# Kernel optimization log

Hardware: AMD Instinct MI355X
Metric: run time of the kernel (lower is better)

Reference implementation:

```python
import jax, jax.numpy as jnp
import numpy as np

ATOM_FDIM, BOND_FDIM, HID, DEPTH = 133, 147, 256, 4
N_ATOMS, N_BONDS, MAX_NB, A_PER_MOL = 4096, 8192, 6, 64


def _ln(x, g, b, eps=1e-5):
    mu = x.mean(-1, keepdims=True)
    var = ((x - mu) ** 2).mean(-1, keepdims=True)
    return (x - mu) / jnp.sqrt(var + eps) * g + b


def setup_inputs() -> dict:
    key = jax.random.key(0)
    ks = jax.random.split(key, 20)
    def w(k, i, o):
        return jax.random.normal(k, (i, o), jnp.float32) / np.sqrt(i).astype(np.float32)
    return {
        "f_atoms": jax.random.normal(ks[0], (N_ATOMS, ATOM_FDIM), jnp.float32),
        "f_bonds": jax.random.normal(ks[1], (N_BONDS, BOND_FDIM), jnp.float32),
        "Wq_atom": w(ks[2], ATOM_FDIM, ATOM_FDIM),
        "Wk_atom": w(ks[3], ATOM_FDIM, ATOM_FDIM),
        "Wv_atom": w(ks[4], ATOM_FDIM, ATOM_FDIM),
        "ln_g": jnp.ones((ATOM_FDIM,), jnp.float32),
        "ln_b": jnp.zeros((ATOM_FDIM,), jnp.float32),
        "Wi": w(ks[5], BOND_FDIM, HID),
        "Wh": w(ks[6], HID, HID),
        "Wq": w(ks[7], HID, HID),
        "Wk": w(ks[8], HID, HID),
        "Wv": w(ks[9], HID, HID),
        "Wa": w(ks[10], HID, HID),
        "Walpha_w": w(ks[11], 2 * HID, 1),
        "Walpha_b": jnp.zeros((1,), jnp.float32),
        "Wo_w": w(ks[12], ATOM_FDIM + HID, HID),
        "Wo_b": jnp.zeros((HID,), jnp.float32),
        "Wb_w": w(ks[13], HID, HID),
        "Wb_b": jnp.zeros((HID,), jnp.float32),
        "a2b": jax.random.randint(ks[14], (N_ATOMS, MAX_NB), 0, N_BONDS),
        "b2a": jax.random.randint(ks[15], (N_BONDS,), 0, N_ATOMS),
        "b2revb": jax.random.randint(ks[16], (N_BONDS,), 0, N_BONDS),
        "atoms_per_mol": A_PER_MOL,
    }


def reference(f_atoms, f_bonds, Wq_atom, Wk_atom, Wv_atom, ln_g, ln_b, Wi, Wh,
              Wq, Wk, Wv, Wa, Walpha_w, Walpha_b, Wo_w, Wo_b, Wb_w, Wb_b,
              a2b, b2a, b2revb, atoms_per_mol):
    M = f_atoms.shape[0] // atoms_per_mol
    fdim = f_atoms.shape[1]
    # --- per-molecule atom self-attention enhancement (uniform a_scope) ---
    x = f_atoms.reshape(M, atoms_per_mol, fdim)  # [M, A, F]
    q, k, v = x @ Wq_atom, x @ Wk_atom, x @ Wv_atom
    scores = jnp.einsum('maf,mbf->mab', q, k) / np.sqrt(fdim).astype(np.float32)
    attn_out = jnp.einsum('mab,mbf->maf', jax.nn.softmax(scores, -1), v)
    f_atoms_e = _ln(x + attn_out, ln_g, ln_b).reshape(-1, fdim)

    # --- bond message init ---
    inputs = f_bonds @ Wi                      # [B, H]
    message = jax.nn.relu(inputs)
    sqrt_h = np.sqrt(HID).astype(np.float32)

    for _ in range(DEPTH - 1):
        # DMPNN gather-sum
        a_message = message[a2b].sum(1)        # [N_atoms, H]
        dmpnn = (a_message[b2a] - message[b2revb]) @ Wh
        # global bond-bond attention (faithful to torch: over all messages)
        Q, K, V = message @ Wq, message @ Wk, message @ Wv
        att_w = jax.nn.softmax(Q @ K.T / sqrt_h, -1)   # [B, B]
        att_msg = (att_w @ V) @ Wa
        alpha = jax.nn.sigmoid(
            jnp.concatenate([dmpnn, att_msg], -1) @ Walpha_w + Walpha_b)
        message = jax.nn.relu(inputs + alpha * dmpnn + (1.0 - alpha) * att_msg)
        # dropout is identity in eval mode

    # --- atom readout ---
    a_message = message[a2b].sum(1)
    a_input = jnp.concatenate([f_atoms_e, a_message], 1)
    atom_h = jax.nn.relu(a_input @ Wo_w + Wo_b)        # [N_atoms, H]

    # --- per-molecule attentive pooling ---
    hm = atom_h.reshape(M, atoms_per_mol, HID)
    aw = jax.nn.softmax(jnp.einsum('mah,mbh->mab', hm @ Wa, hm), -1)
    att_h = jax.nn.relu(jnp.einsum('mab,mbh->mah', aw, hm) @ Wb_w + Wb_b)
    mol_vecs = (hm + att_h).sum(1) / atoms_per_mol
    return mol_vecs
```

## Files before the change

kernel.cpp:

```cpp
#include <hip/hip_runtime.h>
#include <hip/hip_bf16.h>

typedef __hip_bfloat16 hbf16;
typedef __bf16 bf16x8 __attribute__((ext_vector_type(8)));
typedef float floatx4 __attribute__((ext_vector_type(4)));

#define N_ATOMS 4096
#define N_BONDS 8192
#define FDIM 133
#define BFDIM 147
#define HID 256
#define APM 64
#define NMOL 64
#define FA_S 160
#define FB_S 160
#define AI_S 416

struct P4 { float* p[4]; };
struct CvtTab { const void* src[6]; float* dst[6]; int n[6]; };
struct WTab { const void* src[11]; hbf16* dst[11]; int K[11]; int Hout[11]; int Kp[11]; int total[11]; };

__device__ __forceinline__ float bcvt(hbf16 x) { return __bfloat162float(x); }

__device__ __forceinline__ float load_in(const void* src, int i, int f32flag)
{
    return f32flag ? ((const float*)src)[i] : bcvt(((const hbf16*)src)[i]);
}

__device__ __forceinline__ void split8(const float4 a0, const float4 a1,
                                       bf16x8& hi, bf16x8& lo)
{
    const float v[8] = {a0.x, a0.y, a0.z, a0.w, a1.x, a1.y, a1.z, a1.w};
    #pragma unroll
    for (int i = 0; i < 8; i++) {
        const __bf16 h = (__bf16)v[i];
        hi[i] = h;
        lo[i] = (__bf16)(v[i] - (float)h);
    }
}

__global__ void detect_kernel(const unsigned short* __restrict__ probe, int* __restrict__ flag)
{
    const int t = threadIdx.x;
    float mx = 0.f;
    for (int i = t; i < 4096; i += 64) {
        unsigned int u = ((unsigned int)probe[i]) << 16;
        float v;
        __builtin_memcpy(&v, &u, 4);
        v = fabsf(v);
        if (!(v == v)) v = 0.f;
        if (v > 1e6f) v = 1e6f;
        mx = fmaxf(mx, v);
    }
    #pragma unroll
    for (int o = 32; o > 0; o >>= 1) mx = fmaxf(mx, __shfl_xor(mx, o));
    if (t == 0) *flag = (mx > 100.f) ? 1 : 0;
}

__global__ void small_cvt_kernel(CvtTab tab, const int* __restrict__ flag)
{
    const int f32 = *flag;
    for (int s = 0; s < 6; s++)
        for (int i = threadIdx.x; i < tab.n[s]; i += 256)
            tab.dst[s][i] = load_in(tab.src[s], i, f32);
}

__global__ void cvt_pad_kernel(const void* __restrict__ src, float* __restrict__ dst,
                               int N, int K, int Kp, const int* __restrict__ flag)
{
    const int i = blockIdx.x * 256 + threadIdx.x;
    if (i >= N * Kp) return;
    const int r = i / Kp, k = i - r * Kp;
    dst[i] = (k < K) ? load_in(src, r * K + k, *flag) : 0.f;
}

__global__ void wt_all_kernel(WTab tab, const int* __restrict__ flag)
{
    const int wid = blockIdx.y;
    const int f32 = *flag;
    const int tot = tab.total[wid], Kp = tab.Kp[wid], K = tab.K[wid], Hout = tab.Hout[wid];
    hbf16* dst = tab.dst[wid];
    const void* src = tab.src[wid];
    for (int i = blockIdx.x * 256 + threadIdx.x; i < tot; i += gridDim.x * 256) {
        const int n = i / Kp, k = i - n * Kp;
        const float v = (k < K && n < Hout) ? load_in(src, k * Hout + n, f32) : 0.f;
        dst[i] = __float2bfloat16(v);
    }
}

__global__ __launch_bounds__(256)
void mgemm_kernel(const float* __restrict__ A, int lda, const hbf16* __restrict__ Wt,
                  const float* __restrict__ bias,
                  float* __restrict__ Cf, float* __restrict__ Cf2, int ldcf,
                  hbf16* __restrict__ Cbh, hbf16* __restrict__ Cbl, int ldcb,
                  hbf16* __restrict__ CbT, int ldct,
                  int Hout, int HoutStore, int relu)
{
    const int t = threadIdx.x, w = t >> 6, ln = t & 63;
    const int lane16 = ln & 15, quad = ln >> 4;
    const int rb = blockIdx.y * 64 + w * 16, cb = blockIdx.x * 64;
    const floatx4 zero4 = {0.f, 0.f, 0.f, 0.f};
    floatx4 acc[4] = {zero4, zero4, zero4, zero4};
    const float* ar = A + (size_t)(rb + lane16) * lda + quad * 8;
    for (int kk = 0; kk < lda; kk += 32) {
        const float4 a0 = *(const float4*)(ar + kk);
        const float4 a1 = *(const float4*)(ar + kk + 4);
        bf16x8 af;
        af[0] = (__bf16)a0.x; af[1] = (__bf16)a0.y; af[2] = (__bf16)a0.z; af[3] = (__bf16)a0.w;
        af[4] = (__bf16)a1.x; af[5] = (__bf16)a1.y; af[6] = (__bf16)a1.z; af[7] = (__bf16)a1.w;
        #pragma unroll
        for (int nt = 0; nt < 4; nt++) {
            const bf16x8 bf =
                *(const bf16x8*)&Wt[(size_t)(cb + nt * 16 + lane16) * lda + kk + quad * 8];
            acc[nt] = __builtin_amdgcn_mfma_f32_16x16x32_bf16(af, bf, acc[nt], 0, 0, 0);
        }
    }
    #pragma unroll
    for (int nt = 0; nt < 4; nt++) {
        const int n = cb + nt * 16 + lane16;
        if (n >= HoutStore) continue;
        const bool valid = n < Hout;
        const float bv = (bias && valid) ? bias[n] : 0.f;
        #pragma unroll
        for (int r = 0; r < 4; r++) {
            const int m = rb + quad * 4 + r;
            float v = valid ? acc[nt][r] + bv : 0.f;
            if (relu) v = fmaxf(v, 0.f);
            if (Cf)  Cf[(size_t)m * ldcf + n] = v;
            if (Cf2) Cf2[(size_t)m * ldcf + n] = fmaxf(v, 0.f);
            if (Cbh) {
                const hbf16 h = __float2bfloat16(v);
                Cbh[(size_t)m * ldcb + n] = h;
                if (Cbl) Cbl[(size_t)m * ldcb + n] = __float2bfloat16(v - bcvt(h));
            }
            if (CbT) CbT[(size_t)n * ldct + m] = __float2bfloat16(v);
        }
    }
}

__global__ __launch_bounds__(256)
void atom_fused_kernel(const float* __restrict__ qa, const float* __restrict__ ka,
                       const hbf16* __restrict__ vT, const float* __restrict__ f_atoms_p,
                       const float* __restrict__ ln_g, const float* __restrict__ ln_b,
                       float* __restrict__ f_e)
{
    __shared__ float S[64][68];
    __shared__ __bf16 P[64][72];
    __shared__ float Y[64][136];
    const int m = blockIdx.x, t = threadIdx.x;
    const int w = t >> 6, ln = t & 63;
    const int lane16 = ln & 15, quad = ln >> 4;
    const int base = m * APM;
    const floatx4 zero4 = {0.f, 0.f, 0.f, 0.f};

    {
        floatx4 acc[4] = {zero4, zero4, zero4, zero4};
        const float* arow = qa + (size_t)(base + w * 16 + lane16) * FA_S + quad * 8;
        #pragma unroll
        for (int ks = 0; ks < 5; ks++) {
            bf16x8 ah, al;
            split8(*(const float4*)(arow + ks * 32), *(const float4*)(arow + ks * 32 + 4), ah, al);
            #pragma unroll
            for (int nt = 0; nt < 4; nt++) {
                const float* brow = ka + (size_t)(base + nt * 16 + lane16) * FA_S + ks * 32 + quad * 8;
                bf16x8 bh, bl;
                split8(*(const float4*)brow, *(const float4*)(brow + 4), bh, bl);
                acc[nt] = __builtin_amdgcn_mfma_f32_16x16x32_bf16(ah, bh, acc[nt], 0, 0, 0);
                acc[nt] = __builtin_amdgcn_mfma_f32_16x16x32_bf16(al, bh, acc[nt], 0, 0, 0);
                acc[nt] = __builtin_amdgcn_mfma_f32_16x16x32_bf16(ah, bl, acc[nt], 0, 0, 0);
            }
        }
        const float scale = 1.f / sqrtf(133.f);
        #pragma unroll
        for (int nt = 0; nt < 4; nt++)
            #pragma unroll
            for (int r = 0; r < 4; r++)
                S[w * 16 + quad * 4 + r][nt * 16 + lane16] = acc[nt][r] * scale;
    }
    for (int r = w * 16; r < w * 16 + 16; r++) {
        const float x = S[r][ln];
        float mx = x;
        #pragma unroll
        for (int o = 32; o > 0; o >>= 1) mx = fmaxf(mx, __shfl_xor(mx, o));
        const float p = __expf(x - mx);
        float sm = p;
        #pragma unroll
        for (int o = 32; o > 0; o >>= 1) sm += __shfl_xor(sm, o);
        P[r][ln] = (__bf16)(p / sm);
    }
    {
        floatx4 o[9];
        #pragma unroll
        for (int i = 0; i < 9; i++) o[i] = zero4;
        #pragma unroll
        for (int ks = 0; ks < 2; ks++) {
            const bf16x8 af = *(const bf16x8*)&P[w * 16 + lane16][ks * 32 + quad * 8];
            #pragma unroll
            for (int nt = 0; nt < 9; nt++) {
                const bf16x8 bfv =
                    *(const bf16x8*)&vT[(size_t)(nt * 16 + lane16) * N_ATOMS + base + ks * 32 + quad * 8];
                o[nt] = __builtin_amdgcn_mfma_f32_16x16x32_bf16(af, bfv, o[nt], 0, 0, 0);
            }
        }
        #pragma unroll
        for (int nt = 0; nt < 9; nt++) {
            const int f = nt * 16 + lane16;
            if (f >= FDIM) continue;
            #pragma unroll
            for (int r = 0; r < 4; r++) {
                const int a = w * 16 + quad * 4 + r;
                Y[a][f] = f_atoms_p[(size_t)(base + a) * FA_S + f] + o[nt][r];
            }
        }
    }
    for (int r = w * 16; r < w * 16 + 16; r++) {
        float sum = 0.f, sq = 0.f;
        for (int f = ln; f < FDIM; f += 64) { const float v = Y[r][f]; sum += v; sq += v * v; }
        #pragma unroll
        for (int o = 32; o > 0; o >>= 1) { sum += __shfl_xor(sum, o); sq += __shfl_xor(sq, o); }
        const float mu = sum / FDIM;
        const float var = sq / FDIM - mu * mu;
        const float rstd = rsqrtf(var + 1e-5f);
        for (int f = ln; f < FDIM; f += 64) {
            const float v = (Y[r][f] - mu) * rstd;
            f_e[(size_t)(base + r) * FDIM + f] = v * ln_g[f] + ln_b[f];
        }
    }
}

__global__ __launch_bounds__(256)
void pool_fused_kernel(const float* __restrict__ hmWa, const float* __restrict__ atom_h,
                       const hbf16* __restrict__ hm_hi, const hbf16* __restrict__ hm_lo,
                       const hbf16* __restrict__ hmT, const hbf16* __restrict__ Wtb,
                       const float* __restrict__ Wb_b, void* __restrict__ out,
                       const int* __restrict__ flag)
{
    __shared__ float S[64][68];
    __shared__ __bf16 P[64][72];
    __shared__ __bf16 att[64][264];
    const int m = blockIdx.x, t = threadIdx.x;
    const int w = t >> 6, ln = t & 63;
    const int lane16 = ln & 15, quad = ln >> 4;
    const int base = m * APM;
    const floatx4 zero4 = {0.f, 0.f, 0.f, 0.f};

    {
        floatx4 acc[4] = {zero4, zero4, zero4, zero4};
        const float* arow = hmWa + (size_t)(base + w * 16 + lane16) * HID + quad * 8;
        #pragma unroll
        for (int ks = 0; ks < 8; ks++) {
            bf16x8 ah, al;
            split8(*(const float4*)(arow + ks * 32), *(const float4*)(arow + ks * 32 + 4), ah, al);
            #pragma unroll
            for (int nt = 0; nt < 4; nt++) {
                const size_t bidx = (size_t)(base + nt * 16 + lane16) * HID + ks * 32 + quad * 8;
                const bf16x8 bh = *(const bf16x8*)&hm_hi[bidx];
                const bf16x8 bl = *(const bf16x8*)&hm_lo[bidx];
                acc[nt] = __builtin_amdgcn_mfma_f32_16x16x32_bf16(ah, bh, acc[nt], 0, 0, 0);
                acc[nt] = __builtin_amdgcn_mfma_f32_16x16x32_bf16(al, bh, acc[nt], 0, 0, 0);
                acc[nt] = __builtin_amdgcn_mfma_f32_16x16x32_bf16(ah, bl, acc[nt], 0, 0, 0);
            }
        }
        #pragma unroll
        for (int nt = 0; nt < 4; nt++)
            #pragma unroll
            for (int r = 0; r < 4; r++)
                S[w * 16 + quad * 4 + r][nt * 16 + lane16] = acc[nt][r];
    }
    for (int r = w * 16; r < w * 16 + 16; r++) {
        const float x = S[r][ln];
        float mx = x;
        #pragma unroll
        for (int o = 32; o > 0; o >>= 1) mx = fmaxf(mx, __shfl_xor(mx, o));
        const float p = __expf(x - mx);
        float sm = p;
        #pragma unroll
        for (int o = 32; o > 0; o >>= 1) sm += __shfl_xor(sm, o);
        P[r][ln] = (__bf16)(p / sm);
    }
    __syncthreads();
    {
        floatx4 o3[4][4];
        #pragma unroll
        for (int mt = 0; mt < 4; mt++)
            #pragma unroll
            for (int nt = 0; nt < 4; nt++) o3[mt][nt] = zero4;
        #pragma unroll
        for (int ks = 0; ks < 2; ks++) {
            bf16x8 af[4];
            #pragma unroll
            for (int mt = 0; mt < 4; mt++)
                af[mt] = *(const bf16x8*)&P[mt * 16 + lane16][ks * 32 + quad * 8];
            #pragma unroll
            for (int nt = 0; nt < 4; nt++) {
                const bf16x8 bfv = *(const bf16x8*)
                    &hmT[(size_t)(w * 64 + nt * 16 + lane16) * N_ATOMS + base + ks * 32 + quad * 8];
                #pragma unroll
                for (int mt = 0; mt < 4; mt++)
                    o3[mt][nt] = __builtin_amdgcn_mfma_f32_16x16x32_bf16(af[mt], bfv, o3[mt][nt], 0, 0, 0);
            }
        }
        #pragma unroll
        for (int mt = 0; mt < 4; mt++)
            #pragma unroll
            for (int nt = 0; nt < 4; nt++)
                #pragma unroll
                for (int r = 0; r < 4; r++)
                    att[mt * 16 + quad * 4 + r][w * 64 + nt * 16 + lane16] = (__bf16)o3[mt][nt][r];
    }
    __syncthreads();
    {
        floatx4 o5[4][4];
        #pragma unroll
        for (int mt = 0; mt < 4; mt++)
            #pragma unroll
            for (int nt = 0; nt < 4; nt++) o5[mt][nt] = zero4;
        #pragma unroll
        for (int ks = 0; ks < 8; ks++) {
            bf16x8 af[4];
            #pragma unroll
            for (int mt = 0; mt < 4; mt++)
                af[mt] = *(const bf16x8*)&att[mt * 16 + lane16][ks * 32 + quad * 8];
            #pragma unroll
            for (int nt = 0; nt < 4; nt++) {
                const bf16x8 bfv = *(const bf16x8*)
                    &Wtb[(size_t)(w * 64 + nt * 16 + lane16) * HID + ks * 32 + quad * 8];
                #pragma unroll
                for (int mt = 0; mt < 4; mt++)
                    o5[mt][nt] = __builtin_amdgcn_mfma_f32_16x16x32_bf16(af[mt], bfv, o5[mt][nt], 0, 0, 0);
            }
        }
        #pragma unroll
        for (int nt = 0; nt < 4; nt++) {
            const int n = w * 64 + nt * 16 + lane16;
            const float bv = Wb_b[n];
            float s = 0.f;
            #pragma unroll
            for (int mt = 0; mt < 4; mt++)
                #pragma unroll
                for (int r = 0; r < 4; r++)
                    s += fmaxf(o5[mt][nt][r] + bv, 0.f);
            s += __shfl_xor(s, 16);
            s += __shfl_xor(s, 32);
            if (quad == 0) {
                float hsum = 0.f;
                for (int a = 0; a < APM; a++)
                    hsum += atom_h[(size_t)(base + a) * HID + n];
                const float v = (s + hsum) * (1.f / 64.f);
                if (*flag) ((float*)out)[m * HID + n] = v;
                else       ((hbf16*)out)[m * HID + n] = __float2bfloat16(v);
            }
        }
    }
}

__global__ __launch_bounds__(256)
void flash_kernel(const hbf16* __restrict__ Qg, const hbf16* __restrict__ Kg,
                  const hbf16* __restrict__ Vtg, P4 parts, float2* __restrict__ ml)
{
    __shared__ __align__(16) __bf16 Ks[32][264];
    __shared__ __align__(16) __bf16 Vt[256][40];
    __shared__ __align__(16) __bf16 Ps[4][16][40];

    const int t = threadIdx.x, w = t >> 6, ln = t & 63;
    const int lane16 = ln & 15, quad = ln >> 4;
    const int cs = blockIdx.x;
    const int rw = blockIdx.y * 64 + w * 16;
    float* __restrict__ part = parts.p[cs];

    bf16x8 qf[8];
    #pragma unroll
    for (int ks = 0; ks < 8; ks++)
        qf[ks] = *(const bf16x8*)&Qg[(size_t)(rw + lane16) * HID + ks * 32 + quad * 8];

    const floatx4 zero4 = {0.f, 0.f, 0.f, 0.f};
    floatx4 O[16];
    #pragma unroll
    for (int i = 0; i < 16; i++) O[i] = zero4;
    float mrow[4] = {-1e30f, -1e30f, -1e30f, -1e30f};
    float lrow[4] = {0.f, 0.f, 0.f, 0.f};
    const float scale = 0.0625f;

    const int cbeg = cs * 2048, cend = cbeg + 2048;
    for (int c0 = cbeg; c0 < cend; c0 += 32) {
        __syncthreads();
        #pragma unroll
        for (int ii = 0; ii < 4; ii++) {
            const int i = t + ii * 256;
            const int row = i >> 5, kc = (i & 31) * 8;
            *(bf16x8*)&Ks[row][kc] = *(const bf16x8*)&Kg[(size_t)(c0 + row) * HID + kc];
        }
        #pragma unroll
        for (int ii = 0; ii < 4; ii++) {
            const int i = t + ii * 256;
            const int row = i >> 2, kc = (i & 3) * 8;
            *(bf16x8*)&Vt[row][kc] = *(const bf16x8*)&Vtg[(size_t)row * N_BONDS + c0 + kc];
        }
        __syncthreads();

        floatx4 s0 = zero4, s1 = zero4;
        #pragma unroll
        for (int ks = 0; ks < 8; ks++) {
            const bf16x8 b0 = *(bf16x8*)&Ks[lane16][ks * 32 + quad * 8];
            const bf16x8 b1 = *(bf16x8*)&Ks[16 + lane16][ks * 32 + quad * 8];
            s0 = __builtin_amdgcn_mfma_f32_16x16x32_bf16(qf[ks], b0, s0, 0, 0, 0);
            s1 = __builtin_amdgcn_mfma_f32_16x16x32_bf16(qf[ks], b1, s1, 0, 0, 0);
        }
        float alpha[4];
        #pragma unroll
        for (int r = 0; r < 4; r++) {
            const float v0 = s0[r] * scale, v1 = s1[r] * scale;
            float mx = fmaxf(v0, v1);
            #pragma unroll
            for (int o = 8; o > 0; o >>= 1) mx = fmaxf(mx, __shfl_xor(mx, o));
            const float mnew = fmaxf(mrow[r], mx);
            const float p0 = __expf(v0 - mnew), p1 = __expf(v1 - mnew);
            float ps = p0 + p1;
            #pragma unroll
            for (int o = 8; o > 0; o >>= 1) ps += __shfl_xor(ps, o);
            alpha[r] = __expf(mrow[r] - mnew);
            lrow[r] = lrow[r] * alpha[r] + ps;
            mrow[r] = mnew;
            const int row = quad * 4 + r;
            Ps[w][row][lane16] = (__bf16)p0;
            Ps[w][row][16 + lane16] = (__bf16)p1;
        }
        #pragma unroll
        for (int nt = 0; nt < 16; nt++)
            #pragma unroll
            for (int r = 0; r < 4; r++) O[nt][r] *= alpha[r];
        const bf16x8 pf = *(bf16x8*)&Ps[w][lane16][quad * 8];
        #pragma unroll
        for (int nt = 0; nt < 16; nt++) {
            const bf16x8 vf = *(bf16x8*)&Vt[nt * 16 + lane16][quad * 8];
            O[nt] = __builtin_amdgcn_mfma_f32_16x16x32_bf16(pf, vf, O[nt], 0, 0, 0);
        }
    }
    #pragma unroll
    for (int r = 0; r < 4; r++) {
        const int row = rw + quad * 4 + r;
        #pragma unroll
        for (int nt = 0; nt < 16; nt++)
            part[(size_t)row * HID + nt * 16 + lane16] = O[nt][r];
        if (lane16 == 0) ml[cs * N_BONDS + row] = make_float2(mrow[r], lrow[r]);
    }
}

__global__ void flash_combine_kernel(P4 parts, const float2* __restrict__ ml,
                                     float* __restrict__ out)
{
    const int row = blockIdx.x, h = threadIdx.x;
    float2 e[4];
    float M = -1e30f;
    #pragma unroll
    for (int i = 0; i < 4; i++) { e[i] = ml[i * N_BONDS + row]; M = fmaxf(M, e[i].x); }
    float den = 0.f, val = 0.f;
    #pragma unroll
    for (int i = 0; i < 4; i++) {
        const float wgt = __expf(e[i].x - M);
        den += wgt * e[i].y;
        val += wgt * parts.p[i][(size_t)row * HID + h];
    }
    out[(size_t)row * HID + h] = val / den;
}

__global__ void gather_kernel(const float* __restrict__ msg, const int* __restrict__ a2b,
                              float* __restrict__ amsg)
{
    const int a = blockIdx.x, h = threadIdx.x;
    float s = 0.f;
    #pragma unroll
    for (int i = 0; i < 6; i++) {
        const int b = a2b[a * 6 + i];
        s += msg[(size_t)b * HID + h];
    }
    amsg[(size_t)a * HID + h] = s;
}

__global__ void pre_kernel(const float* __restrict__ amsg, const float* __restrict__ msg,
                           const int* __restrict__ b2a, const int* __restrict__ b2revb,
                           float* __restrict__ pre)
{
    const int b = blockIdx.x, h = threadIdx.x;
    pre[(size_t)b * HID + h] =
        amsg[(size_t)b2a[b] * HID + h] - msg[(size_t)b2revb[b] * HID + h];
}

__global__ __launch_bounds__(256)
void combine_kernel(const float* __restrict__ inputs, const float* __restrict__ dmpnn,
                    const float* __restrict__ att, const float* __restrict__ ww,
                    const float* __restrict__ wb, float* __restrict__ msg)
{
    const int wv = threadIdx.x >> 6, lnid = threadIdx.x & 63;
    const int row = blockIdx.x * 4 + wv;
    const float* dr = dmpnn + (size_t)row * HID;
    const float* ar = att + (size_t)row * HID;
    float dot = 0.f;
    for (int h = lnid; h < HID; h += 64)
        dot += dr[h] * ww[h] + ar[h] * ww[HID + h];
    #pragma unroll
    for (int o = 32; o > 0; o >>= 1) dot += __shfl_xor(dot, o);
    const float alpha = 1.f / (1.f + __expf(-(dot + wb[0])));
    for (int h = lnid; h < HID; h += 64) {
        const float v = inputs[(size_t)row * HID + h] + alpha * dr[h] + (1.f - alpha) * ar[h];
        msg[(size_t)row * HID + h] = fmaxf(v, 0.f);
    }
}

__global__ void concat_kernel(const float* __restrict__ fe, const float* __restrict__ amsg,
                              float* __restrict__ ai)
{
    const int a = blockIdx.x, t = threadIdx.x;
    for (int f = t; f < FDIM; f += 256) ai[(size_t)a * AI_S + f] = fe[(size_t)a * FDIM + f];
    for (int h = t; h < HID; h += 256) ai[(size_t)a * AI_S + FDIM + h] = amsg[(size_t)a * HID + h];
    for (int z = t; z < AI_S - FDIM - HID; z += 256) ai[(size_t)a * AI_S + FDIM + HID + z] = 0.f;
}

extern "C" void kernel_launch(void* const* d_in, const int* in_sizes, int n_in,
                              void* d_out, int out_size, void* d_ws, size_t ws_size,
                              hipStream_t stream)
{
    const int* a2b    = (const int*)d_in[19];
    const int* b2a    = (const int*)d_in[20];
    const int* b2revb = (const int*)d_in[21];

    float* ws = (float*)d_ws;
    size_t off = 0;
    auto alloc = [&](size_t n) { float* p = ws + off; off += (n + 63) & ~(size_t)63; return p; };
    int* flag = (int*)alloc(64);

    float* ln_g     = alloc(FDIM);
    float* ln_b     = alloc(FDIM);
    float* Walpha_w = alloc(2 * HID);
    float* Walpha_b = alloc(64);
    float* Wo_b     = alloc(HID);
    float* Wb_b     = alloc(HID);
    float* f_atoms_p = alloc((size_t)N_ATOMS * FA_S);
    float* f_bonds_p = alloc((size_t)N_BONDS * FB_S);
    auto balloc = [&](size_t n) { return (hbf16*)alloc((n + 1) / 2); };
    hbf16* Wt_qa = balloc((size_t)192 * FA_S);
    hbf16* Wt_ka = balloc((size_t)192 * FA_S);
    hbf16* Wt_va = balloc((size_t)192 * FA_S);
    hbf16* Wt_i  = balloc((size_t)HID * FB_S);
    hbf16* Wt_h  = balloc((size_t)HID * HID);
    hbf16* Wt_q  = balloc((size_t)HID * HID);
    hbf16* Wt_k  = balloc((size_t)HID * HID);
    hbf16* Wt_v  = balloc((size_t)HID * HID);
    hbf16* Wt_a  = balloc((size_t)HID * HID);
    hbf16* Wt_b  = balloc((size_t)HID * HID);
    hbf16* Wt_o  = balloc((size_t)HID * AI_S);

    float* f_e    = alloc((size_t)N_ATOMS * FDIM);
    float* inputs = alloc((size_t)N_BONDS * HID);
    float* msg    = alloc((size_t)N_BONDS * HID);
    float* buf1   = alloc((size_t)N_BONDS * HID);
    float* buf2   = alloc((size_t)N_BONDS * HID);
    float* buf3   = alloc((size_t)N_BONDS * HID);
    float* buf4   = alloc((size_t)N_BONDS * HID);
    float* pnew   = alloc((size_t)N_BONDS * HID);
    float* amsg   = alloc((size_t)N_ATOMS * HID);
    float2* ml    = (float2*)alloc((size_t)4 * N_BONDS * 2);
    hbf16* Qb  = balloc((size_t)N_BONDS * HID);
    hbf16* Kb  = balloc((size_t)N_BONDS * HID);
    hbf16* Vtg = balloc((size_t)N_BONDS * HID);
    hbf16* vTa = (hbf16*)buf3;

    detect_kernel<<<1, 64, 0, stream>>>((const unsigned short*)d_in[1], flag);

    CvtTab ct;
    ct.src[0] = d_in[5];  ct.dst[0] = ln_g;     ct.n[0] = FDIM;
    ct.src[1] = d_in[6];  ct.dst[1] = ln_b;     ct.n[1] = FDIM;
    ct.src[2] = d_in[13]; ct.dst[2] = Walpha_w; ct.n[2] = 2 * HID;
    ct.src[3] = d_in[14]; ct.dst[3] = Walpha_b; ct.n[3] = 1;
    ct.src[4] = d_in[16]; ct.dst[4] = Wo_b;     ct.n[4] = HID;
    ct.src[5] = d_in[18]; ct.dst[5] = Wb_b;     ct.n[5] = HID;
    small_cvt_kernel<<<1, 256, 0, stream>>>(ct, flag);

    cvt_pad_kernel<<<(N_ATOMS * FA_S + 255) / 256, 256, 0, stream>>>(
        d_in[0], f_atoms_p, N_ATOMS, FDIM, FA_S, flag);
    cvt_pad_kernel<<<(N_BONDS * FB_S + 255) / 256, 256, 0, stream>>>(
        d_in[1], f_bonds_p, N_BONDS, BFDIM, FB_S, flag);

    WTab wt;
    const void* wsrc[11] = {d_in[2], d_in[3], d_in[4], d_in[7], d_in[8], d_in[9],
                            d_in[10], d_in[11], d_in[12], d_in[17], d_in[15]};
    hbf16* wdst[11] = {Wt_qa, Wt_ka, Wt_va, Wt_i, Wt_h, Wt_q, Wt_k, Wt_v, Wt_a, Wt_b, Wt_o};
    const int wK[11]  = {FDIM, FDIM, FDIM, BFDIM, HID, HID, HID, HID, HID, HID, FDIM + HID};
    const int wH[11]  = {FDIM, FDIM, FDIM, HID, HID, HID, HID, HID, HID, HID, HID};
    const int wKp[11] = {FA_S, FA_S, FA_S, FB_S, HID, HID, HID, HID, HID, HID, AI_S};
    const int wHp[11] = {192, 192, 192, HID, HID, HID, HID, HID, HID, HID, HID};
    for (int i = 0; i < 11; i++) {
        wt.src[i] = wsrc[i]; wt.dst[i] = wdst[i]; wt.K[i] = wK[i]; wt.Hout[i] = wH[i];
        wt.Kp[i] = wKp[i]; wt.total[i] = wHp[i] * wKp[i];
    }
    wt_all_kernel<<<dim3(416, 11), 256, 0, stream>>>(wt, flag);

    auto mg = [&](const float* A, int lda, const hbf16* Wt, const float* bias,
                  float* Cf, float* Cf2, int ldcf, hbf16* Cbh, hbf16* Cbl, int ldcb,
                  hbf16* CbT, int ldct, int rows, int Hout, int HoutStore, int relu) {
        dim3 grid((HoutStore + 63) / 64, rows / 64);
        mgemm_kernel<<<grid, 256, 0, stream>>>(A, lda, Wt, bias, Cf, Cf2, ldcf,
                                               Cbh, Cbl, ldcb, CbT, ldct,
                                               Hout, HoutStore, relu);
    };

    mg(f_atoms_p, FA_S, Wt_qa, nullptr, buf1, nullptr, FA_S, nullptr, nullptr, 0,
       nullptr, 0, N_ATOMS, FDIM, FA_S, 0);
    mg(f_atoms_p, FA_S, Wt_ka, nullptr, buf2, nullptr, FA_S, nullptr, nullptr, 0,
       nullptr, 0, N_ATOMS, FDIM, FA_S, 0);
    mg(f_atoms_p, FA_S, Wt_va, nullptr, nullptr, nullptr, 0, nullptr, nullptr, 0,
       vTa, N_ATOMS, N_ATOMS, FDIM, 192, 0);
    atom_fused_kernel<<<NMOL, 256, 0, stream>>>(buf1, buf2, vTa, f_atoms_p, ln_g, ln_b, f_e);

    mg(f_bonds_p, FB_S, Wt_i, nullptr, inputs, msg, HID, nullptr, nullptr, 0,
       nullptr, 0, N_BONDS, HID, HID, 0);

    P4 parts; parts.p[0] = buf1; parts.p[1] = buf3; parts.p[2] = buf4; parts.p[3] = pnew;

    for (int d = 0; d < 3; d++) {
        gather_kernel<<<N_ATOMS, 256, 0, stream>>>(msg, a2b, amsg);
        pre_kernel<<<N_BONDS, 256, 0, stream>>>(amsg, msg, b2a, b2revb, buf1);
        mg(buf1, HID, Wt_h, nullptr, buf2, nullptr, HID, nullptr, nullptr, 0,
           nullptr, 0, N_BONDS, HID, HID, 0);
        mg(msg, HID, Wt_q, nullptr, nullptr, nullptr, 0, Qb, nullptr, HID,
           nullptr, 0, N_BONDS, HID, HID, 0);
        mg(msg, HID, Wt_k, nullptr, nullptr, nullptr, 0, Kb, nullptr, HID,
           nullptr, 0, N_BONDS, HID, HID, 0);
        mg(msg, HID, Wt_v, nullptr, nullptr, nullptr, 0, nullptr, nullptr, 0,
           Vtg, N_BONDS, N_BONDS, HID, HID, 0);
        flash_kernel<<<dim3(4, N_BONDS / 64), 256, 0, stream>>>(Qb, Kb, Vtg, parts, ml);
        flash_combine_kernel<<<N_BONDS, 256, 0, stream>>>(parts, ml, buf3);
        mg(buf3, HID, Wt_a, nullptr, buf4, nullptr, HID, nullptr, nullptr, 0,
           nullptr, 0, N_BONDS, HID, HID, 0);
        combine_kernel<<<N_BONDS / 4, 256, 0, stream>>>(inputs, buf2, buf4, Walpha_w,
                                                        Walpha_b, msg);
    }

    gather_kernel<<<N_ATOMS, 256, 0, stream>>>(msg, a2b, amsg);
    concat_kernel<<<N_ATOMS, 256, 0, stream>>>(f_e, amsg, buf1);
    mg(buf1, AI_S, Wt_o, Wo_b, buf4, nullptr, HID, Qb, Kb, HID,
       Vtg, N_ATOMS, N_ATOMS, HID, HID, 1);

    mg(buf4, HID, Wt_a, nullptr, buf3, nullptr, HID, nullptr, nullptr, 0,
       nullptr, 0, N_ATOMS, HID, HID, 0);
    pool_fused_kernel<<<NMOL, 256, 0, stream>>>(buf3, buf4, Qb, Kb, Vtg, Wt_b,
                                                Wb_b, d_out, flag);
}
```

Before: 1.134 ms.

## Split flash attention into 8 chunks, swizzle LDS, fuse QKV projections

The bond-bond flash attention now splits keys into 8 chunks instead of 4, which doubles grid parallelism, and gets launch bounds for 4 blocks per CU. K and V tiles in shared memory use XOR swizzling in place of padding to avoid bank conflicts. Rescaling of the output accumulator is skipped when no row maximum changed. The three Q/K/V projection GEMMs are merged into one launch with a z-dimension. In exchange, the combine step reads twice as many partial buffers, which adds memory traffic and four extra allocations.

```diff
diff --git a/kernel.cpp b/kernel.cpp
--- a/kernel.cpp
+++ b/kernel.cpp
@@ -15,8 +15,10 @@
 #define FA_S 160
 #define FB_S 160
 #define AI_S 416
-
-struct P4 { float* p[4]; };
+#define CS 8
+
+struct P8 { float* p[8]; };
+struct QKV { const hbf16* w[3]; hbf16* outp[3]; };
 struct CvtTab { const void* src[6]; float* dst[6]; int n[6]; };
 struct WTab { const void* src[11]; hbf16* dst[11]; int K[11]; int Hout[11]; int Kp[11]; int total[11]; };
 
@@ -134,6 +136,44 @@
                 if (Cbl) Cbl[(size_t)m * ldcb + n] = __float2bfloat16(v - bcvt(h));
             }
             if (CbT) CbT[(size_t)n * ldct + m] = __float2bfloat16(v);
+        }
+    }
+}
+
+__global__ __launch_bounds__(256)
+void qkv_kernel(const float* __restrict__ A, QKV q)
+{
+    const int z = blockIdx.z;
+    const hbf16* __restrict__ Wt = q.w[z];
+    hbf16* __restrict__ outp = q.outp[z];
+    const int t = threadIdx.x, w = t >> 6, ln = t & 63;
+    const int lane16 = ln & 15, quad = ln >> 4;
+    const int rb = blockIdx.y * 64 + w * 16, cb = blockIdx.x * 64;
+    const floatx4 zero4 = {0.f, 0.f, 0.f, 0.f};
+    floatx4 acc[4] = {zero4, zero4, zero4, zero4};
+    const float* ar = A + (size_t)(rb + lane16) * HID + quad * 8;
+    for (int kk = 0; kk < HID; kk += 32) {
+        const float4 a0 = *(const float4*)(ar + kk);
+        const float4 a1 = *(const float4*)(ar + kk + 4);
+        bf16x8 af;
+        af[0] = (__bf16)a0.x; af[1] = (__bf16)a0.y; af[2] = (__bf16)a0.z; af[3] = (__bf16)a0.w;
+        af[4] = (__bf16)a1.x; af[5] = (__bf16)a1.y; af[6] = (__bf16)a1.z; af[7] = (__bf16)a1.w;
+        #pragma unroll
+        for (int nt = 0; nt < 4; nt++) {
+            const bf16x8 bf =
+                *(const bf16x8*)&Wt[(size_t)(cb + nt * 16 + lane16) * HID + kk + quad * 8];
+            acc[nt] = __builtin_amdgcn_mfma_f32_16x16x32_bf16(af, bf, acc[nt], 0, 0, 0);
+        }
+    }
+    #pragma unroll
+    for (int nt = 0; nt < 4; nt++) {
+        const int n = cb + nt * 16 + lane16;
+        #pragma unroll
+        for (int r = 0; r < 4; r++) {
+            const int m = rb + quad * 4 + r;
+            const hbf16 h = __float2bfloat16(acc[nt][r]);
+            if (z < 2) outp[(size_t)m * HID + n] = h;
+            else       outp[(size_t)n * N_BONDS + m] = h;
         }
     }
 }
@@ -354,12 +394,12 @@
     }
 }
 
-__global__ __launch_bounds__(256)
+__global__ __launch_bounds__(256, 4)
 void flash_kernel(const hbf16* __restrict__ Qg, const hbf16* __restrict__ Kg,
-                  const hbf16* __restrict__ Vtg, P4 parts, float2* __restrict__ ml)
-{
-    __shared__ __align__(16) __bf16 Ks[32][264];
-    __shared__ __align__(16) __bf16 Vt[256][40];
+                  const hbf16* __restrict__ Vtg, P8 parts, float2* __restrict__ ml)
+{
+    __shared__ __align__(16) __bf16 Ks[32][256];
+    __shared__ __align__(16) __bf16 Vt[256][32];
     __shared__ __align__(16) __bf16 Ps[4][16][40];
 
     const int t = threadIdx.x, w = t >> 6, ln = t & 63;
@@ -381,28 +421,31 @@
     float lrow[4] = {0.f, 0.f, 0.f, 0.f};
     const float scale = 0.0625f;
 
-    const int cbeg = cs * 2048, cend = cbeg + 2048;
+    const int cbeg = cs * (N_BONDS / CS), cend = cbeg + N_BONDS / CS;
     for (int c0 = cbeg; c0 < cend; c0 += 32) {
         __syncthreads();
         #pragma unroll
         for (int ii = 0; ii < 4; ii++) {
-            const int i = t + ii * 256;
-            const int row = i >> 5, kc = (i & 31) * 8;
-            *(bf16x8*)&Ks[row][kc] = *(const bf16x8*)&Kg[(size_t)(c0 + row) * HID + kc];
+            const int idx = t + ii * 256;
+            const int row = idx >> 5, c = idx & 31;
+            *(bf16x8*)&Ks[row][(c ^ (row & 31)) * 8] =
+                *(const bf16x8*)&Kg[(size_t)(c0 + row) * HID + c * 8];
         }
         #pragma unroll
         for (int ii = 0; ii < 4; ii++) {
-            const int i = t + ii * 256;
-            const int row = i >> 2, kc = (i & 3) * 8;
-            *(bf16x8*)&Vt[row][kc] = *(const bf16x8*)&Vtg[(size_t)row * N_BONDS + c0 + kc];
+            const int idx = t + ii * 256;
+            const int row = idx >> 2, c = idx & 3;
+            *(bf16x8*)&Vt[row][(c ^ (row & 3)) * 8] =
+                *(const bf16x8*)&Vtg[(size_t)row * N_BONDS + c0 + c * 8];
         }
         __syncthreads();
 
         floatx4 s0 = zero4, s1 = zero4;
         #pragma unroll
         for (int ks = 0; ks < 8; ks++) {
-            const bf16x8 b0 = *(bf16x8*)&Ks[lane16][ks * 32 + quad * 8];
-            const bf16x8 b1 = *(bf16x8*)&Ks[16 + lane16][ks * 32 + quad * 8];
+            const int ch = ks * 4 + quad;
+            const bf16x8 b0 = *(bf16x8*)&Ks[lane16][(ch ^ lane16) * 8];
+            const bf16x8 b1 = *(bf16x8*)&Ks[16 + lane16][(ch ^ (16 + lane16)) * 8];
             s0 = __builtin_amdgcn_mfma_f32_16x16x32_bf16(qf[ks], b0, s0, 0, 0, 0);
             s1 = __builtin_amdgcn_mfma_f32_16x16x32_bf16(qf[ks], b1, s1, 0, 0, 0);
         }
@@ -425,14 +468,18 @@
             Ps[w][row][lane16] = (__bf16)p0;
             Ps[w][row][16 + lane16] = (__bf16)p1;
         }
-        #pragma unroll
-        for (int nt = 0; nt < 16; nt++)
-            #pragma unroll
-            for (int r = 0; r < 4; r++) O[nt][r] *= alpha[r];
+        const bool need = (alpha[0] < 1.f) | (alpha[1] < 1.f) | (alpha[2] < 1.f) | (alpha[3] < 1.f);
+        if (__any(need)) {
+            #pragma unroll
+            for (int nt = 0; nt < 16; nt++)
+                #pragma unroll
+                for (int r = 0; r < 4; r++) O[nt][r] *= alpha[r];
+        }
         const bf16x8 pf = *(bf16x8*)&Ps[w][lane16][quad * 8];
         #pragma unroll
         for (int nt = 0; nt < 16; nt++) {
-            const bf16x8 vf = *(bf16x8*)&Vt[nt * 16 + lane16][quad * 8];
+            const int vrow = nt * 16 + lane16;
+            const bf16x8 vf = *(bf16x8*)&Vt[vrow][(quad ^ (vrow & 3)) * 8];
             O[nt] = __builtin_amdgcn_mfma_f32_16x16x32_bf16(pf, vf, O[nt], 0, 0, 0);
         }
     }
@@ -446,17 +493,17 @@
     }
 }
 
-__global__ void flash_combine_kernel(P4 parts, const float2* __restrict__ ml,
+__global__ void flash_combine_kernel(P8 parts, const float2* __restrict__ ml,
                                      float* __restrict__ out)
 {
     const int row = blockIdx.x, h = threadIdx.x;
-    float2 e[4];
+    float2 e[CS];
     float M = -1e30f;
     #pragma unroll
-    for (int i = 0; i < 4; i++) { e[i] = ml[i * N_BONDS + row]; M = fmaxf(M, e[i].x); }
+    for (int i = 0; i < CS; i++) { e[i] = ml[i * N_BONDS + row]; M = fmaxf(M, e[i].x); }
     float den = 0.f, val = 0.f;
     #pragma unroll
-    for (int i = 0; i < 4; i++) {
+    for (int i = 0; i < CS; i++) {
         const float wgt = __expf(e[i].x - M);
         den += wgt * e[i].y;
         val += wgt * parts.p[i][(size_t)row * HID + h];
@@ -558,8 +605,12 @@
     float* buf3   = alloc((size_t)N_BONDS * HID);
     float* buf4   = alloc((size_t)N_BONDS * HID);
     float* pnew   = alloc((size_t)N_BONDS * HID);
+    float* pext0  = alloc((size_t)N_BONDS * HID);
+    float* pext1  = alloc((size_t)N_BONDS * HID);
+    float* pext2  = alloc((size_t)N_BONDS * HID);
+    float* pext3  = alloc((size_t)N_BONDS * HID);
     float* amsg   = alloc((size_t)N_ATOMS * HID);
-    float2* ml    = (float2*)alloc((size_t)4 * N_BONDS * 2);
+    float2* ml    = (float2*)alloc((size_t)CS * N_BONDS * 2);
     hbf16* Qb  = balloc((size_t)N_BONDS * HID);
     hbf16* Kb  = balloc((size_t)N_BONDS * HID);
     hbf16* Vtg = balloc((size_t)N_BONDS * HID);
@@ -615,20 +666,20 @@
     mg(f_bonds_p, FB_S, Wt_i, nullptr, inputs, msg, HID, nullptr, nullptr, 0,
        nullptr, 0, N_BONDS, HID, HID, 0);
 
-    P4 parts; parts.p[0] = buf1; parts.p[1] = buf3; parts.p[2] = buf4; parts.p[3] = pnew;
+    P8 parts;
+    parts.p[0] = buf1; parts.p[1] = buf3; parts.p[2] = buf4; parts.p[3] = pnew;
+    parts.p[4] = pext0; parts.p[5] = pext1; parts.p[6] = pext2; parts.p[7] = pext3;
+    QKV qkv;
+    qkv.w[0] = Wt_q; qkv.w[1] = Wt_k; qkv.w[2] = Wt_v;
+    qkv.outp[0] = Qb; qkv.outp[1] = Kb; qkv.outp[2] = Vtg;
 
     for (int d = 0; d < 3; d++) {
         gather_kernel<<<N_ATOMS, 256, 0, stream>>>(msg, a2b, amsg);
         pre_kernel<<<N_BONDS, 256, 0, stream>>>(amsg, msg, b2a, b2revb, buf1);
         mg(buf1, HID, Wt_h, nullptr, buf2, nullptr, HID, nullptr, nullptr, 0,
            nullptr, 0, N_BONDS, HID, HID, 0);
-        mg(msg, HID, Wt_q, nullptr, nullptr, nullptr, 0, Qb, nullptr, HID,
-           nullptr, 0, N_BONDS, HID, HID, 0);
-        mg(msg, HID, Wt_k, nullptr, nullptr, nullptr, 0, Kb, nullptr, HID,
-           nullptr, 0, N_BONDS, HID, HID, 0);
-        mg(msg, HID, Wt_v, nullptr, nullptr, nullptr, 0, nullptr, nullptr, 0,
-           Vtg, N_BONDS, N_BONDS, HID, HID, 0);
-        flash_kernel<<<dim3(4, N_BONDS / 64), 256, 0, stream>>>(Qb, Kb, Vtg, parts, ml);
+        qkv_kernel<<<dim3(4, N_BONDS / 64, 3), 256, 0, stream>>>(msg, qkv);
+        flash_kernel<<<dim3(CS, N_BONDS / 64), 256, 0, stream>>>(Qb, Kb, Vtg, parts, ml);
         flash_combine_kernel<<<N_BONDS, 256, 0, stream>>>(parts, ml, buf3);
         mg(buf3, HID, Wt_a, nullptr, buf4, nullptr, HID, nullptr, nullptr, 0,
            nullptr, 0, N_BONDS, HID, HID, 0);
```

After: 1.694 ms. +49.4%, slower.
